# Optimization experiments

Measured on AMD Instinct MI355X. Metric: run time of the kernel, lower is better.

Reference implementation:

```python
import jax, jax.numpy as jnp
import numpy as np

H = 2048
V = 50257
M = 64

def setup_inputs() -> dict:
    key = jax.random.key(0)
    ks = jax.random.split(key, 14)
    s = 0.02  # weight init scale for numerical sanity
    return {
        "input_tok": jax.random.randint(ks[0], (1,), 0, V),
        "hidden": jax.random.normal(ks[1], (1, 1, H), jnp.float32),
        "encoder_outputs": jax.random.normal(ks[2], (M, H), jnp.float32),
        "emb": jax.random.normal(ks[3], (V, H), jnp.float32) * s,
        "attn_w": jax.random.normal(ks[4], (M, 2 * H), jnp.float32) * s,
        "attn_b": jax.random.normal(ks[5], (M,), jnp.float32) * s,
        "comb_w": jax.random.normal(ks[6], (H, 2 * H), jnp.float32) * s,
        "comb_b": jax.random.normal(ks[7], (H,), jnp.float32) * s,
        "w_ih": jax.random.normal(ks[8], (3 * H, H), jnp.float32) * s,
        "w_hh": jax.random.normal(ks[9], (3 * H, H), jnp.float32) * s,
        "b_ih": jax.random.normal(ks[10], (3 * H,), jnp.float32) * s,
        "b_hh": jax.random.normal(ks[11], (3 * H,), jnp.float32) * s,
        "out_w": jax.random.normal(ks[12], (V, H), jnp.float32) * s,
        "out_b": jax.random.normal(ks[13], (V,), jnp.float32) * s,
    }

def reference(input_tok, hidden, encoder_outputs, emb, attn_w, attn_b,
              comb_w, comb_b, w_ih, w_hh, b_ih, b_hh, out_w, out_b):
    # embedded: [1, H] (dropout is eval-mode identity)
    embedded = emb[input_tok].reshape(1, H)
    h0 = hidden[0]  # [1, H]
    # Bahdanau-style attention over encoder outputs
    attn_weights = jax.nn.softmax(
        jnp.concatenate([embedded, h0], axis=1) @ attn_w.T + attn_b, axis=1)  # [1, M]
    attn_applied = attn_weights @ encoder_outputs  # [1, H]
    # combine + relu
    x = jnp.concatenate([embedded, attn_applied], axis=1) @ comb_w.T + comb_b
    x = jax.nn.relu(x)  # [1, H] -> GRU input
    # single GRU cell step, PyTorch gate order (r, z, n)
    gi = x @ w_ih.T + b_ih   # [1, 3H]
    gh = h0 @ w_hh.T + b_hh  # [1, 3H]
    i_r, i_z, i_n = jnp.split(gi, 3, axis=1)
    h_r, h_z, h_n = jnp.split(gh, 3, axis=1)
    r = jax.nn.sigmoid(i_r + h_r)
    z = jax.nn.sigmoid(i_z + h_z)
    n = jnp.tanh(i_n + r * h_n)
    h_new = (1.0 - z) * n + z * h0  # [1, H]
    # output projection + log-softmax over vocab
    log_probs = jax.nn.log_softmax(h_new @ out_w.T + out_b, axis=1)  # [1, V]
    return (log_probs, h_new[None], attn_weights)
```

## Files before the change

kernel.cpp:

```cpp
#include <hip/hip_runtime.h>
#include <math.h>

#define H 2048
#define V 50257
#define M 64

__device__ inline float wred_sum(float v) {
#pragma unroll
    for (int o = 32; o >= 1; o >>= 1) v += __shfl_down(v, o);
    return v;
}

__global__ void k_scores(const int* __restrict__ tok, const float* __restrict__ hidden,
                         const float* __restrict__ emb, const float* __restrict__ attn_w,
                         const float* __restrict__ attn_b, float* __restrict__ scores) {
    const int m = blockIdx.x;
    const int t = threadIdx.x;
    const float* erow = emb + (size_t)tok[0] * H;
    const float4* w4 = (const float4*)(attn_w + (size_t)m * 2 * H);
    float acc = 0.f;
    for (int i = t; i < 1024; i += 256) {
        float4 w = w4[i];
        int k = i * 4;
        float4 c = (k < H) ? *(const float4*)(erow + k)
                           : *(const float4*)(hidden + (k - H));
        acc += w.x * c.x + w.y * c.y + w.z * c.z + w.w * c.w;
    }
    __shared__ float sred[4];
    float s = wred_sum(acc);
    int wid = t >> 6, lane = t & 63;
    if (lane == 0) sred[wid] = s;
    __syncthreads();
    if (t == 0) scores[m] = sred[0] + sred[1] + sred[2] + sred[3] + attn_b[m];
}

__global__ void k_softmax_m(const float* __restrict__ scores, float* __restrict__ aw_out) {
    int lane = threadIdx.x;
    float s = scores[lane];
    float mx = s;
#pragma unroll
    for (int o = 32; o >= 1; o >>= 1) mx = fmaxf(mx, __shfl_xor(mx, o));
    float e = expf(s - mx);
    float sum = e;
#pragma unroll
    for (int o = 32; o >= 1; o >>= 1) sum += __shfl_xor(sum, o);
    aw_out[lane] = e / sum;
}

__global__ void k_attn_applied(const float* __restrict__ aw, const float* __restrict__ enc,
                               float* __restrict__ attn_applied) {
    int h = blockIdx.x * 256 + threadIdx.x;
    __shared__ float w[M];
    if (threadIdx.x < M) w[threadIdx.x] = aw[threadIdx.x];
    __syncthreads();
    float acc = 0.f;
#pragma unroll 8
    for (int m = 0; m < M; ++m) acc += w[m] * enc[(size_t)m * H + h];
    attn_applied[h] = acc;
}

__global__ void k_combine(const int* __restrict__ tok, const float* __restrict__ emb,
                          const float* __restrict__ comb_w, const float* __restrict__ comb_b,
                          const float* __restrict__ aa, float* __restrict__ x_out) {
    int r = (blockIdx.x * blockDim.x + threadIdx.x) >> 6;
    int lane = threadIdx.x & 63;
    const float* erow = emb + (size_t)tok[0] * H;
    const float4* w4 = (const float4*)(comb_w + (size_t)r * 2 * H);
    float acc = 0.f;
#pragma unroll
    for (int it = 0; it < 16; ++it) {
        int i = it * 64 + lane;
        float4 w = w4[i];
        int k = i * 4;
        float4 c = (k < H) ? *(const float4*)(erow + k)
                           : *(const float4*)(aa + (k - H));
        acc += w.x * c.x + w.y * c.y + w.z * c.z + w.w * c.w;
    }
    acc = wred_sum(acc);
    if (lane == 0) x_out[r] = fmaxf(acc + comb_b[r], 0.f);
}

__global__ void k_gru(const float* __restrict__ hidden, const float* __restrict__ w_ih,
                      const float* __restrict__ w_hh, const float* __restrict__ b_ih,
                      const float* __restrict__ b_hh, const float* __restrict__ x,
                      float* __restrict__ h_out) {
    int j = (blockIdx.x * blockDim.x + threadIdx.x) >> 6;
    int lane = threadIdx.x & 63;
    const float4* x4 = (const float4*)x;
    const float4* h4 = (const float4*)hidden;
    const float4* wir = (const float4*)(w_ih + (size_t)j * H);
    const float4* wiz = (const float4*)(w_ih + (size_t)(H + j) * H);
    const float4* win = (const float4*)(w_ih + (size_t)(2 * H + j) * H);
    const float4* whr = (const float4*)(w_hh + (size_t)j * H);
    const float4* whz = (const float4*)(w_hh + (size_t)(H + j) * H);
    const float4* whn = (const float4*)(w_hh + (size_t)(2 * H + j) * H);
    float air = 0, aiz = 0, ain = 0, ahr = 0, ahz = 0, ahn = 0;
#pragma unroll
    for (int it = 0; it < 8; ++it) {
        int i = it * 64 + lane;
        float4 xv = x4[i], hv = h4[i];
        float4 a;
        a = wir[i]; air += a.x * xv.x + a.y * xv.y + a.z * xv.z + a.w * xv.w;
        a = wiz[i]; aiz += a.x * xv.x + a.y * xv.y + a.z * xv.z + a.w * xv.w;
        a = win[i]; ain += a.x * xv.x + a.y * xv.y + a.z * xv.z + a.w * xv.w;
        a = whr[i]; ahr += a.x * hv.x + a.y * hv.y + a.z * hv.z + a.w * hv.w;
        a = whz[i]; ahz += a.x * hv.x + a.y * hv.y + a.z * hv.z + a.w * hv.w;
        a = whn[i]; ahn += a.x * hv.x + a.y * hv.y + a.z * hv.z + a.w * hv.w;
    }
    air = wred_sum(air); aiz = wred_sum(aiz); ain = wred_sum(ain);
    ahr = wred_sum(ahr); ahz = wred_sum(ahz); ahn = wred_sum(ahn);
    if (lane == 0) {
        float r = 1.f / (1.f + expf(-(air + b_ih[j] + ahr + b_hh[j])));
        float z = 1.f / (1.f + expf(-(aiz + b_ih[H + j] + ahz + b_hh[H + j])));
        float n = tanhf(ain + b_ih[2 * H + j] + r * (ahn + b_hh[2 * H + j]));
        h_out[j] = (1.f - z) * n + z * hidden[j];
    }
}

__global__ void k_logits(const float* __restrict__ out_w, const float* __restrict__ out_b,
                         const float* __restrict__ hnew, float* __restrict__ logits) {
    int v = (blockIdx.x * blockDim.x + threadIdx.x) >> 6;
    if (v >= V) return;
    int lane = threadIdx.x & 63;
    const float4* w4 = (const float4*)(out_w + (size_t)v * H);
    const float4* h4 = (const float4*)hnew;
    float acc = 0.f;
#pragma unroll
    for (int it = 0; it < 8; ++it) {
        int i = it * 64 + lane;
        float4 w = w4[i], h = h4[i];
        acc += w.x * h.x + w.y * h.y + w.z * h.z + w.w * h.w;
    }
    acc = wred_sum(acc);
    if (lane == 0) logits[v] = acc + out_b[v];
}

__global__ void k_lse_part(const float* __restrict__ logits, float* __restrict__ part) {
    int t = threadIdx.x, b = blockIdx.x;
    float m = -INFINITY, s = 0.f;
    for (int i = b * 256 + t; i < V; i += 64 * 256) {
        float v = logits[i];
        if (v > m) { s = s * expf(m - v) + 1.f; m = v; }
        else s += expf(v - m);
    }
    __shared__ float sm[256], ss[256];
    sm[t] = m; ss[t] = s;
    __syncthreads();
    for (int o = 128; o >= 1; o >>= 1) {
        if (t < o) {
            float m2 = sm[t + o], s2 = ss[t + o];
            float mm = fmaxf(sm[t], m2);
            ss[t] = ss[t] * expf(sm[t] - mm) + s2 * expf(m2 - mm);
            sm[t] = mm;
        }
        __syncthreads();
    }
    if (t == 0) { part[b] = sm[0]; part[64 + b] = ss[0]; }
}

__global__ void k_lse_final(const float* __restrict__ part, float* __restrict__ g) {
    int lane = threadIdx.x;
    float m = part[lane], s = part[64 + lane];
#pragma unroll
    for (int o = 32; o >= 1; o >>= 1) {
        float m2 = __shfl_xor(m, o), s2 = __shfl_xor(s, o);
        float mm = fmaxf(m, m2);
        s = s * expf(m - mm) + s2 * expf(m2 - mm);
        m = mm;
    }
    if (lane == 0) { g[0] = m; g[1] = logf(s); }
}

__global__ void k_logsoftmax(float* __restrict__ logits, const float* __restrict__ g) {
    int i = blockIdx.x * 256 + threadIdx.x;
    if (i < V) logits[i] = logits[i] - g[0] - g[1];
}

extern "C" void kernel_launch(void* const* d_in, const int* in_sizes, int n_in,
                              void* d_out, int out_size, void* d_ws, size_t ws_size,
                              hipStream_t stream) {
    const int*   tok     = (const int*)d_in[0];
    const float* hidden  = (const float*)d_in[1];
    const float* enc     = (const float*)d_in[2];
    const float* emb     = (const float*)d_in[3];
    const float* attn_w  = (const float*)d_in[4];
    const float* attn_b  = (const float*)d_in[5];
    const float* comb_w  = (const float*)d_in[6];
    const float* comb_b  = (const float*)d_in[7];
    const float* w_ih    = (const float*)d_in[8];
    const float* w_hh    = (const float*)d_in[9];
    const float* b_ih    = (const float*)d_in[10];
    const float* b_hh    = (const float*)d_in[11];
    const float* out_w   = (const float*)d_in[12];
    const float* out_b   = (const float*)d_in[13];

    float* out = (float*)d_out;
    float* logp  = out;
    float* hout  = out + V;
    float* awout = out + V + H;

    float* ws   = (float*)d_ws;
    float* AA   = ws;
    float* X    = ws + 2048;
    float* SC   = ws + 4096;
    float* PART = ws + 4160;
    float* G    = ws + 4288;

    k_scores      <<<64,    256, 0, stream>>>(tok, hidden, emb, attn_w, attn_b, SC);
    k_softmax_m   <<<1,     64,  0, stream>>>(SC, awout);
    k_attn_applied<<<8,     256, 0, stream>>>(awout, enc, AA);
    k_combine     <<<512,   256, 0, stream>>>(tok, emb, comb_w, comb_b, AA, X);
    k_gru         <<<512,   256, 0, stream>>>(hidden, w_ih, w_hh, b_ih, b_hh, X, hout);
    k_logits      <<<12565, 256, 0, stream>>>(out_w, out_b, hout, logp);
    k_lse_part    <<<64,    256, 0, stream>>>(logp, PART);
    k_lse_final   <<<1,     64,  0, stream>>>(PART, G);
    k_logsoftmax  <<<197,   256, 0, stream>>>(logp, G);
}
```

Before: 120.1 us.

## Fuse softmax into attention apply and LSE partials into logits kernel

Merges the attention softmax into the attention-apply kernel, which each block recomputes redundantly. Folds the online log-sum-exp partials into the logits GEMV, with each wave handling 13 vocab rows and caching h in registers. The final reduction moves into the normalize kernel, where every block re-reduces 967 partials. This cuts the chain from nine launches to six and skips a separate pass over the logits, at the cost of redundant per-block reductions and fewer, heavier logits blocks.

```diff
diff --git a/kernel.cpp b/kernel.cpp
--- a/kernel.cpp
+++ b/kernel.cpp
@@ -4,6 +4,12 @@
 #define H 2048
 #define V 50257
 #define M 64
+
+#define NEG_BIG (-1.0e30f)
+
+#define RPW 13
+#define NB5 967
+#define NB6 197
 
 __device__ inline float wred_sum(float v) {
 #pragma unroll
@@ -34,25 +40,25 @@
     if (t == 0) scores[m] = sred[0] + sred[1] + sred[2] + sred[3] + attn_b[m];
 }
 
-__global__ void k_softmax_m(const float* __restrict__ scores, float* __restrict__ aw_out) {
-    int lane = threadIdx.x;
-    float s = scores[lane];
-    float mx = s;
-#pragma unroll
-    for (int o = 32; o >= 1; o >>= 1) mx = fmaxf(mx, __shfl_xor(mx, o));
-    float e = expf(s - mx);
-    float sum = e;
-#pragma unroll
-    for (int o = 32; o >= 1; o >>= 1) sum += __shfl_xor(sum, o);
-    aw_out[lane] = e / sum;
-}
-
-__global__ void k_attn_applied(const float* __restrict__ aw, const float* __restrict__ enc,
-                               float* __restrict__ attn_applied) {
-    int h = blockIdx.x * 256 + threadIdx.x;
+__global__ void k_sm_aa(const float* __restrict__ scores, const float* __restrict__ enc,
+                        float* __restrict__ aw_out, float* __restrict__ attn_applied) {
     __shared__ float w[M];
-    if (threadIdx.x < M) w[threadIdx.x] = aw[threadIdx.x];
-    __syncthreads();
+    int t = threadIdx.x;
+    if (t < 64) {
+        float s = scores[t];
+        float mx = s;
+#pragma unroll
+        for (int o = 32; o >= 1; o >>= 1) mx = fmaxf(mx, __shfl_xor(mx, o));
+        float e = expf(s - mx);
+        float sum = e;
+#pragma unroll
+        for (int o = 32; o >= 1; o >>= 1) sum += __shfl_xor(sum, o);
+        float aw = e / sum;
+        w[t] = aw;
+        if (blockIdx.x == 0) aw_out[t] = aw;
+    }
+    __syncthreads();
+    int h = blockIdx.x * 256 + t;
     float acc = 0.f;
 #pragma unroll 8
     for (int m = 0; m < M; ++m) acc += w[m] * enc[(size_t)m * H + h];
@@ -118,30 +124,62 @@
 }
 
 __global__ void k_logits(const float* __restrict__ out_w, const float* __restrict__ out_b,
-                         const float* __restrict__ hnew, float* __restrict__ logits) {
-    int v = (blockIdx.x * blockDim.x + threadIdx.x) >> 6;
-    if (v >= V) return;
-    int lane = threadIdx.x & 63;
-    const float4* w4 = (const float4*)(out_w + (size_t)v * H);
+                         const float* __restrict__ hnew, float* __restrict__ logits,
+                         float2* __restrict__ part) {
+    const int t = threadIdx.x;
+    const int lane = t & 63, wid = t >> 6;
+    const int gw = blockIdx.x * 4 + wid;
+    const int base = gw * RPW;
+
     const float4* h4 = (const float4*)hnew;
-    float acc = 0.f;
-#pragma unroll
-    for (int it = 0; it < 8; ++it) {
-        int i = it * 64 + lane;
-        float4 w = w4[i], h = h4[i];
-        acc += w.x * h.x + w.y * h.y + w.z * h.z + w.w * h.w;
-    }
-    acc = wred_sum(acc);
-    if (lane == 0) logits[v] = acc + out_b[v];
-}
-
-__global__ void k_lse_part(const float* __restrict__ logits, float* __restrict__ part) {
-    int t = threadIdx.x, b = blockIdx.x;
-    float m = -INFINITY, s = 0.f;
-    for (int i = b * 256 + t; i < V; i += 64 * 256) {
-        float v = logits[i];
-        if (v > m) { s = s * expf(m - v) + 1.f; m = v; }
-        else s += expf(v - m);
+    float4 h[8];
+#pragma unroll
+    for (int it = 0; it < 8; ++it) h[it] = h4[it * 64 + lane];
+
+    float m = NEG_BIG, s = 0.f;
+#pragma unroll
+    for (int r = 0; r < RPW; ++r) {
+        int row = base + r;
+        if (row >= V) break;
+        const float4* w4 = (const float4*)(out_w + (size_t)row * H);
+        float acc = 0.f;
+#pragma unroll
+        for (int it = 0; it < 8; ++it) {
+            float4 w = w4[it * 64 + lane];
+            acc += w.x * h[it].x + w.y * h[it].y + w.z * h[it].z + w.w * h[it].w;
+        }
+        acc = wred_sum(acc);
+        if (lane == 0) {
+            float lg = acc + out_b[row];
+            logits[row] = lg;
+            if (lg > m) { s = s * expf(m - lg) + 1.f; m = lg; }
+            else s += expf(lg - m);
+        }
+    }
+    __shared__ float2 lms[4];
+    if (lane == 0) lms[wid] = make_float2(m, s);
+    __syncthreads();
+    if (t == 0) {
+        float gm = NEG_BIG, gs = 0.f;
+#pragma unroll
+        for (int i = 0; i < 4; ++i) {
+            float m2 = lms[i].x, s2 = lms[i].y;
+            float mm = fmaxf(gm, m2);
+            gs = gs * expf(gm - mm) + s2 * expf(m2 - mm);
+            gm = mm;
+        }
+        part[blockIdx.x] = make_float2(gm, gs);
+    }
+}
+
+__global__ void k_logsoftmax(float* __restrict__ logits, const float2* __restrict__ part) {
+    const int t = threadIdx.x;
+    float m = NEG_BIG, s = 0.f;
+    for (int i = t; i < NB5; i += 256) {
+        float2 p = part[i];
+        float mm = fmaxf(m, p.x);
+        s = s * expf(m - mm) + p.y * expf(p.x - mm);
+        m = mm;
     }
     __shared__ float sm[256], ss[256];
     sm[t] = m; ss[t] = s;
@@ -155,25 +193,9 @@
         }
         __syncthreads();
     }
-    if (t == 0) { part[b] = sm[0]; part[64 + b] = ss[0]; }
-}
-
-__global__ void k_lse_final(const float* __restrict__ part, float* __restrict__ g) {
-    int lane = threadIdx.x;
-    float m = part[lane], s = part[64 + lane];
-#pragma unroll
-    for (int o = 32; o >= 1; o >>= 1) {
-        float m2 = __shfl_xor(m, o), s2 = __shfl_xor(s, o);
-        float mm = fmaxf(m, m2);
-        s = s * expf(m - mm) + s2 * expf(m2 - mm);
-        m = mm;
-    }
-    if (lane == 0) { g[0] = m; g[1] = logf(s); }
-}
-
-__global__ void k_logsoftmax(float* __restrict__ logits, const float* __restrict__ g) {
-    int i = blockIdx.x * 256 + threadIdx.x;
-    if (i < V) logits[i] = logits[i] - g[0] - g[1];
+    float lse = sm[0] + logf(ss[0]);
+    int i = blockIdx.x * 256 + t;
+    if (i < V) logits[i] -= lse;
 }
 
 extern "C" void kernel_launch(void* const* d_in, const int* in_sizes, int n_in,
@@ -200,19 +222,15 @@
     float* awout = out + V + H;
 
     float* ws   = (float*)d_ws;
-    float* AA   = ws;
-    float* X    = ws + 2048;
-    float* SC   = ws + 4096;
-    float* PART = ws + 4160;
-    float* G    = ws + 4288;
-
-    k_scores      <<<64,    256, 0, stream>>>(tok, hidden, emb, attn_w, attn_b, SC);
-    k_softmax_m   <<<1,     64,  0, stream>>>(SC, awout);
-    k_attn_applied<<<8,     256, 0, stream>>>(awout, enc, AA);
-    k_combine     <<<512,   256, 0, stream>>>(tok, emb, comb_w, comb_b, AA, X);
-    k_gru         <<<512,   256, 0, stream>>>(hidden, w_ih, w_hh, b_ih, b_hh, X, hout);
-    k_logits      <<<12565, 256, 0, stream>>>(out_w, out_b, hout, logp);
-    k_lse_part    <<<64,    256, 0, stream>>>(logp, PART);
-    k_lse_final   <<<1,     64,  0, stream>>>(PART, G);
-    k_logsoftmax  <<<197,   256, 0, stream>>>(logp, G);
-}
+    float*  AA   = ws;
+    float*  X    = ws + 2048;
+    float*  SC   = ws + 4096;
+    float2* PART = (float2*)(ws + 4224);
+
+    k_scores    <<<64,  256, 0, stream>>>(tok, hidden, emb, attn_w, attn_b, SC);
+    k_sm_aa     <<<8,   256, 0, stream>>>(SC, enc, awout, AA);
+    k_combine   <<<512, 256, 0, stream>>>(tok, emb, comb_w, comb_b, AA, X);
+    k_gru       <<<512, 256, 0, stream>>>(hidden, w_ih, w_hh, b_ih, b_hh, X, hout);
+    k_logits    <<<NB5, 256, 0, stream>>>(out_w, out_b, hout, logp, PART);
+    k_logsoftmax<<<NB6, 256, 0, stream>>>(logp, PART);
+}
```

Result: slower. 122.9 us (+2.3%).
